# Kernel optimization log

Hardware: AMD Instinct MI355X
Metric: run time of the kernel (lower is better)

Reference implementation:

```python
import jax, jax.numpy as jnp
import numpy as np

DIM = 512
HEADS = 8
D_HEAD = 64
INNER_FF = 4 * DIM  # 2048
EPS = 1e-5
SCALE = D_HEAD ** -0.5


def _layernorm(x, w, b):
    x = x.astype(jnp.float32)
    mu = jnp.mean(x, axis=-1, keepdims=True)
    var = jnp.mean(jnp.square(x - mu), axis=-1, keepdims=True)
    return (x - mu) * jax.lax.rsqrt(var + EPS) * w + b


def _l2_attn(x, wq, bq, wv, bv, wo, bo):
    # x: [B, N, DIM]. k = q (context is ignored in the original module).
    b, n, _ = x.shape
    q = (x @ wq + bq).reshape(b, n, HEADS, D_HEAD).transpose(0, 2, 1, 3)  # b h n d
    v = (x @ wv + bv).reshape(b, n, HEADS, D_HEAD).transpose(0, 2, 1, 3)
    q = q.astype(jnp.float32)
    AB = jnp.einsum('bhid,bhjd->bhij', q, q)          # [b,h,n,n]
    AA = jnp.sum(jnp.square(q), axis=-1)               # [b,h,n]
    sim = -(AA[..., :, None] - 2.0 * AB + AA[..., None, :]) * SCALE
    attn = jax.nn.softmax(sim, axis=-1)
    out = jnp.einsum('bhij,bhjd->bhid', attn, v)       # [b,h,n,d]
    out = out.transpose(0, 2, 1, 3).reshape(b, n, HEADS * D_HEAD)
    return out @ wo + bo


def _geglu_ff(x, w1, b1, w2, b2):
    h = x @ w1 + b1                      # [B, N, 2*INNER_FF]
    a, gate = jnp.split(h, 2, axis=-1)
    return (a * jax.nn.gelu(gate, approximate=False)) @ w2 + b2


def setup_inputs() -> dict:
    key = jax.random.key(0)
    ks = jax.random.split(key, 24)
    s = 0.02
    d = {'x': jax.random.normal(ks[0], (4, 2048, DIM), jnp.float32)}
    # layernorms
    d['sa_norm_w'] = jnp.ones((DIM,), jnp.float32)
    d['sa_norm_b'] = jnp.zeros((DIM,), jnp.float32)
    d['ca_norm_w'] = jnp.ones((DIM,), jnp.float32)
    d['ca_norm_b'] = jnp.zeros((DIM,), jnp.float32)
    d['ff_norm_w'] = jnp.ones((DIM,), jnp.float32)
    d['ff_norm_b'] = jnp.zeros((DIM,), jnp.float32)
    # attn1 (self)
    d['a1_wq'] = jax.random.normal(ks[1], (DIM, DIM), jnp.float32) * s
    d['a1_bq'] = jnp.zeros((DIM,), jnp.float32)
    d['a1_wv'] = jax.random.normal(ks[2], (DIM, DIM), jnp.float32) * s
    d['a1_bv'] = jnp.zeros((DIM,), jnp.float32)
    d['a1_wo'] = jax.random.normal(ks[3], (DIM, DIM), jnp.float32) * s
    d['a1_bo'] = jnp.zeros((DIM,), jnp.float32)
    # attn2 (cross, but k=q and v from x in original code)
    d['a2_wq'] = jax.random.normal(ks[4], (DIM, DIM), jnp.float32) * s
    d['a2_bq'] = jnp.zeros((DIM,), jnp.float32)
    d['a2_wv'] = jax.random.normal(ks[5], (DIM, DIM), jnp.float32) * s
    d['a2_bv'] = jnp.zeros((DIM,), jnp.float32)
    d['a2_wo'] = jax.random.normal(ks[6], (DIM, DIM), jnp.float32) * s
    d['a2_bo'] = jnp.zeros((DIM,), jnp.float32)
    # GEGLU FFN
    d['ff_w1'] = jax.random.normal(ks[7], (DIM, 2 * INNER_FF), jnp.float32) * s
    d['ff_b1'] = jnp.zeros((2 * INNER_FF,), jnp.float32)
    d['ff_w2'] = jax.random.normal(ks[8], (INNER_FF, DIM), jnp.float32) * s
    d['ff_b2'] = jnp.zeros((DIM,), jnp.float32)
    return d


def reference(x, sa_norm_w, sa_norm_b, ca_norm_w, ca_norm_b, ff_norm_w, ff_norm_b,
              a1_wq, a1_bq, a1_wv, a1_bv, a1_wo, a1_bo,
              a2_wq, a2_bq, a2_wv, a2_bv, a2_wo, a2_bo,
              ff_w1, ff_b1, ff_w2, ff_b2):
    x = _l2_attn(_layernorm(x, sa_norm_w, sa_norm_b), a1_wq, a1_bq, a1_wv, a1_bv, a1_wo, a1_bo) + x
    x = _l2_attn(_layernorm(x, ca_norm_w, ca_norm_b), a2_wq, a2_bq, a2_wv, a2_bv, a2_wo, a2_bo) + x
    x = _geglu_ff(_layernorm(x, ff_norm_w, ff_norm_b), ff_w1, ff_b1, ff_w2, ff_b2) + x
    return x
```

## Files before the change

### kernel.cpp

```cpp
#include <hip/hip_runtime.h>
#include <hip/hip_bf16.h>


typedef short bf16x8 __attribute__((ext_vector_type(8)));
typedef float f32x4 __attribute__((ext_vector_type(4)));
typedef unsigned short u16;
typedef unsigned int u32;

__device__ __forceinline__ float bf2f(u16 u) {
    return __uint_as_float(((u32)u) << 16);
}
__device__ __forceinline__ u16 f2bf(float f) {
    u32 u = __float_as_uint(f);
    u32 rb = ((u >> 16) & 1u) + 0x7fffu;
    return (u16)((u + rb) >> 16);
}
__device__ __forceinline__ float gelu_fast(float x) {
    float y = 1.5957691216f * (x + 0.044715f * x * x * x);
    return x / (1.f + __expf(-y));
}
__device__ __forceinline__ void gl2lds16(const u16* g, u16* l) {
    __builtin_amdgcn_global_load_lds(
        (const __attribute__((address_space(1))) void*)(unsigned long long)(uintptr_t)g,
        (__attribute__((address_space(3))) void*)(unsigned long long)(uintptr_t)l,
        16, 0, 0);
}

struct TArgs {
    const float* src[8];
    u16* dst[8];
    int R[8], C[8];
    int start[9];
};
__global__ __launch_bounds__(256) void transpose_multi(TArgs a) {
    __shared__ float tile[32][33];
    int bid = blockIdx.x;
    int s = 0;
    while (bid >= a.start[s + 1]) s++;
    int local = bid - a.start[s];
    int R = a.R[s], C = a.C[s];
    int tx = C >> 5;
    int bx = local % tx, by = local / tx;
    const float* in = a.src[s];
    u16* out = a.dst[s];
    int t = threadIdx.x;
    int c = t & 31, r0 = (t >> 5) * 4;
#pragma unroll
    for (int i = 0; i < 4; i++)
        tile[r0 + i][c] = in[(size_t)(by * 32 + r0 + i) * C + bx * 32 + c];
    __syncthreads();
#pragma unroll
    for (int i = 0; i < 4; i++)
        out[(size_t)(bx * 32 + r0 + i) * R + by * 32 + c] = f2bf(tile[c][r0 + i]);
}

__global__ __launch_bounds__(256) void ln_kernel(const float* __restrict__ x,
                                                 const float* __restrict__ w,
                                                 const float* __restrict__ b,
                                                 u16* __restrict__ out) {
    int t = threadIdx.x;
    int wave = t >> 6, lane = t & 63;
    int row = blockIdx.x * 4 + wave;
    const float* xr = x + (size_t)row * 512 + lane * 8;
    float4 v0 = *(const float4*)xr;
    float4 v1 = *(const float4*)(xr + 4);
    float s1 = (v0.x + v0.y) + (v0.z + v0.w) + (v1.x + v1.y) + (v1.z + v1.w);
    float s2 = (v0.x * v0.x + v0.y * v0.y) + (v0.z * v0.z + v0.w * v0.w) +
               (v1.x * v1.x + v1.y * v1.y) + (v1.z * v1.z + v1.w * v1.w);
#pragma unroll
    for (int m = 1; m < 64; m <<= 1) {
        s1 += __shfl_xor(s1, m);
        s2 += __shfl_xor(s2, m);
    }
    float mu = s1 * (1.f / 512.f);
    float var = s2 * (1.f / 512.f) - mu * mu;
    float rs = rsqrtf(var + 1e-5f);
    const float* wp = w + lane * 8;
    const float* bp = b + lane * 8;
    float4 w0 = *(const float4*)wp;
    float4 w1 = *(const float4*)(wp + 4);
    float4 b0 = *(const float4*)bp;
    float4 b1 = *(const float4*)(bp + 4);
    u16 r[8];
    r[0] = f2bf((v0.x - mu) * rs * w0.x + b0.x);
    r[1] = f2bf((v0.y - mu) * rs * w0.y + b0.y);
    r[2] = f2bf((v0.z - mu) * rs * w0.z + b0.z);
    r[3] = f2bf((v0.w - mu) * rs * w0.w + b0.w);
    r[4] = f2bf((v1.x - mu) * rs * w1.x + b1.x);
    r[5] = f2bf((v1.y - mu) * rs * w1.y + b1.y);
    r[6] = f2bf((v1.z - mu) * rs * w1.z + b1.z);
    r[7] = f2bf((v1.w - mu) * rs * w1.w + b1.w);
    *(uint4*)(out + (size_t)row * 512 + lane * 8) = *(uint4*)r;
}

__global__ __launch_bounds__(256) void gemm_ff1(const u16* __restrict__ A,
                                                const u16* __restrict__ BT,
                                                const float* __restrict__ bias,
                                                u16* __restrict__ gout,
                                                int K) {
    __shared__ u16 As[2][128 * 32];
    __shared__ u16 Bs[2][128 * 32];
    int t = threadIdx.x;
    int wave = t >> 6, lane = t & 63, quad = lane >> 4, l16 = lane & 15;
    int m0 = blockIdx.x * 128, n0 = blockIdx.y * 64;
    f32x4 aacc[2][4], gacc[2][4];
#pragma unroll
    for (int i = 0; i < 2; i++)
#pragma unroll
        for (int j = 0; j < 4; j++) {
            aacc[i][j] = (f32x4){0.f, 0.f, 0.f, 0.f};
            gacc[i][j] = (f32x4){0.f, 0.f, 0.f, 0.f};
        }
    const u16* Ag = A + (size_t)(m0 + wave * 32 + (lane >> 2)) * K + (lane & 3) * 8;
    int brow = (wave < 2) ? (n0 + wave * 32) : (2048 + n0 + (wave - 2) * 32);
    const u16* Bg = BT + (size_t)(brow + (lane >> 2)) * K + (lane & 3) * 8;
    int lo = wave * 32 * 32;
    const size_t rstep = (size_t)16 * K;
    gl2lds16(Ag, &As[0][lo]);
    gl2lds16(Ag + rstep, &As[0][lo + 16 * 32]);
    gl2lds16(Bg, &Bs[0][lo]);
    gl2lds16(Bg + rstep, &Bs[0][lo + 16 * 32]);
    int buf = 0;
    for (int k0 = 0; k0 < K; k0 += 32, buf ^= 1) {
        int kn = (k0 + 32 < K) ? (k0 + 32) : k0;
        int nb = buf ^ 1;
        asm volatile("s_waitcnt lgkmcnt(0)\n\ts_barrier" ::: "memory");
        gl2lds16(Ag + kn, &As[nb][lo]);
        gl2lds16(Ag + kn + rstep, &As[nb][lo + 16 * 32]);
        gl2lds16(Bg + kn, &Bs[nb][lo]);
        gl2lds16(Bg + kn + rstep, &Bs[nb][lo + 16 * 32]);
        asm volatile("s_waitcnt vmcnt(4)\n\ts_barrier" ::: "memory");
        bf16x8 a[2];
#pragma unroll
        for (int i = 0; i < 2; i++)
            a[i] = *(const bf16x8*)&As[buf][(wave * 32 + i * 16 + l16) * 32 + quad * 8];
#pragma unroll
        for (int j = 0; j < 4; j++) {
            bf16x8 ba = *(const bf16x8*)&Bs[buf][(j * 16 + l16) * 32 + quad * 8];
            bf16x8 bg = *(const bf16x8*)&Bs[buf][(64 + j * 16 + l16) * 32 + quad * 8];
#pragma unroll
            for (int i = 0; i < 2; i++) {
                aacc[i][j] = __builtin_amdgcn_mfma_f32_16x16x32_bf16(a[i], ba, aacc[i][j], 0, 0, 0);
                gacc[i][j] = __builtin_amdgcn_mfma_f32_16x16x32_bf16(a[i], bg, gacc[i][j], 0, 0, 0);
            }
        }
    }
    asm volatile("s_waitcnt vmcnt(0)" ::: "memory");
    int row_base = m0 + wave * 32 + quad * 4;
#pragma unroll
    for (int j = 0; j < 4; j++) {
        int col = n0 + j * 16 + l16;
        float ba = bias[col];
        float bg = bias[2048 + col];
#pragma unroll
        for (int i = 0; i < 2; i++) {
#pragma unroll
            for (int r = 0; r < 4; r++) {
                int row = row_base + i * 16 + r;
                float av = aacc[i][j][r] + ba;
                float gv = gacc[i][j][r] + bg;
                gout[(size_t)row * 2048 + col] = f2bf(av * gelu_fast(gv));
            }
        }
    }
}

__global__ __launch_bounds__(256) void gemm_qv(const u16* __restrict__ A,
                                               const u16* __restrict__ BT,
                                               const float* __restrict__ bias,
                                               const float* __restrict__ bias2,
                                               u16* __restrict__ outb,
                                               u16* __restrict__ outb2,
                                               float* __restrict__ aa,
                                               int K) {
    __shared__ u16 As[2][128 * 32];
    __shared__ u16 Bs[2][128 * 32];
    int t = threadIdx.x;
    int wave = t >> 6, lane = t & 63, quad = lane >> 4, l16 = lane & 15;
    int m0 = blockIdx.x * 128, n0 = blockIdx.y * 128;
    f32x4 acc[2][8];
#pragma unroll
    for (int i = 0; i < 2; i++)
#pragma unroll
        for (int j = 0; j < 8; j++) acc[i][j] = (f32x4){0.f, 0.f, 0.f, 0.f};
    const u16* Ag = A + (size_t)(m0 + wave * 32 + (lane >> 2)) * K + (lane & 3) * 8;
    const u16* Bg = BT + (size_t)(n0 + wave * 32 + (lane >> 2)) * K + (lane & 3) * 8;
    int lo = wave * 32 * 32;
    const size_t rstep = (size_t)16 * K;
    gl2lds16(Ag, &As[0][lo]);
    gl2lds16(Ag + rstep, &As[0][lo + 16 * 32]);
    gl2lds16(Bg, &Bs[0][lo]);
    gl2lds16(Bg + rstep, &Bs[0][lo + 16 * 32]);
    int buf = 0;
    for (int k0 = 0; k0 < K; k0 += 32, buf ^= 1) {
        int kn = (k0 + 32 < K) ? (k0 + 32) : k0;
        int nb = buf ^ 1;
        asm volatile("s_waitcnt lgkmcnt(0)\n\ts_barrier" ::: "memory");
        gl2lds16(Ag + kn, &As[nb][lo]);
        gl2lds16(Ag + kn + rstep, &As[nb][lo + 16 * 32]);
        gl2lds16(Bg + kn, &Bs[nb][lo]);
        gl2lds16(Bg + kn + rstep, &Bs[nb][lo + 16 * 32]);
        asm volatile("s_waitcnt vmcnt(4)\n\ts_barrier" ::: "memory");
        bf16x8 a[2];
#pragma unroll
        for (int i = 0; i < 2; i++)
            a[i] = *(const bf16x8*)&As[buf][(wave * 32 + i * 16 + l16) * 32 + quad * 8];
#pragma unroll
        for (int j = 0; j < 8; j++) {
            bf16x8 b = *(const bf16x8*)&Bs[buf][(j * 16 + l16) * 32 + quad * 8];
#pragma unroll
            for (int i = 0; i < 2; i++)
                acc[i][j] = __builtin_amdgcn_mfma_f32_16x16x32_bf16(a[i], b, acc[i][j], 0, 0, 0);
        }
    }
    asm volatile("s_waitcnt vmcnt(0)" ::: "memory");
    int row_base = m0 + wave * 32 + quad * 4;
    bool isq = (n0 < 512);
    float ssq[2][2][4];
#pragma unroll
    for (int jh = 0; jh < 2; jh++)
#pragma unroll
        for (int i = 0; i < 2; i++)
#pragma unroll
            for (int r = 0; r < 4; r++) ssq[jh][i][r] = 0.f;
#pragma unroll
    for (int j = 0; j < 8; j++) {
        int col = n0 + j * 16 + l16;
        float bv = isq ? bias[col] : bias2[col - 512];
        int jh = j >> 2;
#pragma unroll
        for (int i = 0; i < 2; i++) {
            int rowA = row_base + i * 16;
            if (isq) {
                int hh = col >> 6, d = col & 63;
#pragma unroll
                for (int r = 0; r < 4; r++) {
                    int row = rowA + r;
                    float v = acc[i][j][r] + bv;
                    ssq[jh][i][r] += v * v;
                    outb[((size_t)((row >> 11) * 8 + hh) * 2048 + (row & 2047)) * 64 + d] = f2bf(v);
                }
            } else {
                int c2 = col - 512;
                int hh = c2 >> 6, d = c2 & 63;
                int n = rowA & 2047;
                int a4 = (n >> 2) & 7;
                int ncol = (n & ~31) + ((a4 & 3) << 3) + ((a4 >> 2) << 2);
                u32 plo = (u32)f2bf(acc[i][j][0] + bv) | ((u32)f2bf(acc[i][j][1] + bv) << 16);
                u32 phi = (u32)f2bf(acc[i][j][2] + bv) | ((u32)f2bf(acc[i][j][3] + bv) << 16);
                uint2 pk; pk.x = plo; pk.y = phi;
                *(uint2*)&outb2[((size_t)((rowA >> 11) * 8 + hh) * 64 + d) * 2048 + ncol] = pk;
            }
        }
    }
    if (isq) {
#pragma unroll
        for (int jh = 0; jh < 2; jh++) {
            int hh = (n0 >> 6) + jh;
#pragma unroll
            for (int i = 0; i < 2; i++) {
#pragma unroll
                for (int r = 0; r < 4; r++) {
                    float s = ssq[jh][i][r];
                    s += __shfl_xor(s, 1); s += __shfl_xor(s, 2);
                    s += __shfl_xor(s, 4); s += __shfl_xor(s, 8);
                    if (l16 == 0) {
                        int row = row_base + i * 16 + r;
                        aa[(size_t)((row >> 11) * 8 + hh) * 2048 + (row & 2047)] = s * 0.18033688f;
                    }
                }
            }
        }
    }
}

template <int MODE>
__global__ __launch_bounds__(256) void gemm_rect(const u16* __restrict__ A,
                                                 const u16* __restrict__ BT,
                                                 const float* __restrict__ bias,
                                                 const float* __restrict__ res,
                                                 float* __restrict__ outf,
                                                 int M, int N, int K) {
    __shared__ u16 As[2][128 * 32];
    __shared__ u16 Bs[2][64 * 32];
    int t = threadIdx.x;
    int wave = t >> 6, lane = t & 63, quad = lane >> 4, l16 = lane & 15;
    int m0 = blockIdx.x * 128, n0 = blockIdx.y * 64;
    f32x4 acc[2][4];
#pragma unroll
    for (int i = 0; i < 2; i++)
#pragma unroll
        for (int j = 0; j < 4; j++) acc[i][j] = (f32x4){0.f, 0.f, 0.f, 0.f};
    const u16* Ag = A + (size_t)(m0 + wave * 32 + (lane >> 2)) * K + (lane & 3) * 8;
    const u16* Bg = BT + (size_t)(n0 + wave * 16 + (lane >> 2)) * K + (lane & 3) * 8;
    int loA = wave * 32 * 32;
    int loB = wave * 16 * 32;
    const size_t rstep = (size_t)16 * K;
    gl2lds16(Ag, &As[0][loA]);
    gl2lds16(Ag + rstep, &As[0][loA + 16 * 32]);
    gl2lds16(Bg, &Bs[0][loB]);
    int buf = 0;
    for (int k0 = 0; k0 < K; k0 += 32, buf ^= 1) {
        int kn = (k0 + 32 < K) ? (k0 + 32) : k0;
        int nb = buf ^ 1;
        asm volatile("s_waitcnt lgkmcnt(0)\n\ts_barrier" ::: "memory");
        gl2lds16(Ag + kn, &As[nb][loA]);
        gl2lds16(Ag + kn + rstep, &As[nb][loA + 16 * 32]);
        gl2lds16(Bg + kn, &Bs[nb][loB]);
        asm volatile("s_waitcnt vmcnt(3)\n\ts_barrier" ::: "memory");
        bf16x8 a[2], b[4];
#pragma unroll
        for (int i = 0; i < 2; i++)
            a[i] = *(const bf16x8*)&As[buf][(wave * 32 + i * 16 + l16) * 32 + quad * 8];
#pragma unroll
        for (int j = 0; j < 4; j++)
            b[j] = *(const bf16x8*)&Bs[buf][(j * 16 + l16) * 32 + quad * 8];
#pragma unroll
        for (int i = 0; i < 2; i++)
#pragma unroll
            for (int j = 0; j < 4; j++)
                acc[i][j] = __builtin_amdgcn_mfma_f32_16x16x32_bf16(a[i], b[j], acc[i][j], 0, 0, 0);
    }
    asm volatile("s_waitcnt vmcnt(0)" ::: "memory");
    int row_base = m0 + wave * 32 + quad * 4;
#pragma unroll
    for (int j = 0; j < 4; j++) {
        int col = n0 + j * 16 + l16;
        float bv = bias[col];
#pragma unroll
        for (int i = 0; i < 2; i++) {
            int rowA = row_base + i * 16;
#pragma unroll
            for (int r = 0; r < 4; r++) {
                size_t idx = (size_t)(rowA + r) * N + col;
                outf[idx] = acc[i][j][r] + bv + res[idx];
            }
        }
    }
}

__global__ __launch_bounds__(256) void attn_mfma(const u16* __restrict__ qbuf,
                                                 const u16* __restrict__ vtp,
                                                 const float* __restrict__ aas,
                                                 u16* __restrict__ out) {
    __shared__ u16 L[2][16384];
    int bid = blockIdx.x;
    int bh = bid & 31;
    int itile = bid >> 5;
    const u16* qb = qbuf + (size_t)bh * 2048 * 64;
    const u16* vtb = vtp + (size_t)bh * 64 * 2048;
    const float* aab = aas + (size_t)bh * 2048;
    int t = threadIdx.x;
    int wave = t >> 6, lane = t & 63, quad = lane >> 4, l16 = lane & 15;
    int sw7 = l16 & 7;
    int ibase = itile * 128 + wave * 32;

    bf16x8 qf[2][2];
    f32x4 O[2][4];
    float lr[2] = {0.f, 0.f};
#pragma unroll
    for (int st = 0; st < 2; st++) {
        const u16* qr = qb + (size_t)(ibase + st * 16 + l16) * 64;
        qf[st][0] = *(const bf16x8*)(qr + quad * 8);
        qf[st][1] = *(const bf16x8*)(qr + 32 + quad * 8);
#pragma unroll
        for (int nt = 0; nt < 4; nt++) O[st][nt] = (f32x4){0.f, 0.f, 0.f, 0.f};
    }

    int qrow[4], qcs[4], qwof[4], vrow[4], vsl[4], vwof[4];
#pragma unroll
    for (int k = 0; k < 4; k++) {
        int s = t + k * 256;
        qrow[k] = s >> 3; qcs[k] = s & 7;
        qwof[k] = qrow[k] * 64 + 8 * (qcs[k] ^ (qrow[k] & 7));
        vrow[k] = s >> 4; vsl[k] = s & 15;
        vwof[k] = 8192 + vrow[k] * 128 + 8 * ((vsl[k] & 8) | ((vsl[k] & 7) ^ (vrow[k] & 7)));
    }
#pragma unroll
    for (int k = 0; k < 4; k++) {
        *(uint4*)&L[0][qwof[k]] = *(const uint4*)(qb + (size_t)qrow[k] * 64 + qcs[k] * 8);
        *(uint4*)&L[0][vwof[k]] = *(const uint4*)(vtb + (size_t)vrow[k] * 2048 + vsl[k] * 8);
    }
    __syncthreads();

    const float C0 = 0.36067376f;
    for (int it = 0; it < 16; ++it) {
        int cur = it & 1;
        int j0 = it << 7;
        uint4 pq[4], pv[4];
        bool more = (it + 1 < 16);
        if (more) {
            int j0n = j0 + 128;
#pragma unroll
            for (int k = 0; k < 4; k++) {
                pq[k] = *(const uint4*)(qb + (size_t)(j0n + qrow[k]) * 64 + qcs[k] * 8);
                pv[k] = *(const uint4*)(vtb + (size_t)vrow[k] * 2048 + j0n + vsl[k] * 8);
            }
        }
        const u16* Q = &L[cur][0];
        const u16* V = &L[cur][8192];
#pragma unroll
        for (int c = 0; c < 4; c++) {
            int r10 = c * 32 + l16, r20 = c * 32 + 16 + l16;
            bf16x8 a10 = *(const bf16x8*)&Q[r10 * 64 + 8 * (quad ^ sw7)];
            bf16x8 a11 = *(const bf16x8*)&Q[r10 * 64 + 8 * ((4 + quad) ^ sw7)];
            bf16x8 a20 = *(const bf16x8*)&Q[r20 * 64 + 8 * (quad ^ sw7)];
            bf16x8 a21 = *(const bf16x8*)&Q[r20 * 64 + 8 * ((4 + quad) ^ sw7)];
            f32x4 s0[2], s1[2];
            __builtin_amdgcn_s_setprio(1);
#pragma unroll
            for (int st = 0; st < 2; st++) {
                f32x4 z = {0.f, 0.f, 0.f, 0.f};
                s0[st] = __builtin_amdgcn_mfma_f32_16x16x32_bf16(a10, qf[st][0], z, 0, 0, 0);
                s0[st] = __builtin_amdgcn_mfma_f32_16x16x32_bf16(a11, qf[st][1], s0[st], 0, 0, 0);
                s1[st] = __builtin_amdgcn_mfma_f32_16x16x32_bf16(a20, qf[st][0], z, 0, 0, 0);
                s1[st] = __builtin_amdgcn_mfma_f32_16x16x32_bf16(a21, qf[st][1], s1[st], 0, 0, 0);
            }
            __builtin_amdgcn_s_setprio(0);
            float4 aav0 = *(const float4*)(aab + j0 + c * 32 + quad * 4);
            float4 aav1 = *(const float4*)(aab + j0 + c * 32 + 16 + quad * 4);
            bf16x8 pa[2];
#pragma unroll
            for (int st = 0; st < 2; st++) {
                float p0 = __builtin_amdgcn_exp2f(fmaf(s0[st][0], C0, -aav0.x));
                float p1 = __builtin_amdgcn_exp2f(fmaf(s0[st][1], C0, -aav0.y));
                float p2 = __builtin_amdgcn_exp2f(fmaf(s0[st][2], C0, -aav0.z));
                float p3 = __builtin_amdgcn_exp2f(fmaf(s0[st][3], C0, -aav0.w));
                float p4 = __builtin_amdgcn_exp2f(fmaf(s1[st][0], C0, -aav1.x));
                float p5 = __builtin_amdgcn_exp2f(fmaf(s1[st][1], C0, -aav1.y));
                float p6 = __builtin_amdgcn_exp2f(fmaf(s1[st][2], C0, -aav1.z));
                float p7 = __builtin_amdgcn_exp2f(fmaf(s1[st][3], C0, -aav1.w));
                lr[st] += (p0 + p1 + p2 + p3) + (p4 + p5 + p6 + p7);
                u32* pu = (u32*)&pa[st];
                pu[0] = __builtin_amdgcn_perm(__float_as_uint(p1), __float_as_uint(p0), 0x07060302u);
                pu[1] = __builtin_amdgcn_perm(__float_as_uint(p3), __float_as_uint(p2), 0x07060302u);
                pu[2] = __builtin_amdgcn_perm(__float_as_uint(p5), __float_as_uint(p4), 0x07060302u);
                pu[3] = __builtin_amdgcn_perm(__float_as_uint(p7), __float_as_uint(p6), 0x07060302u);
            }
            __builtin_amdgcn_s_setprio(1);
#pragma unroll
            for (int nt = 0; nt < 4; nt++) {
                int sl = c * 4 + quad;
                bf16x8 vf = *(const bf16x8*)&V[(nt * 16 + l16) * 128 + 8 * ((sl & 8) | ((sl & 7) ^ sw7))];
                O[0][nt] = __builtin_amdgcn_mfma_f32_16x16x32_bf16(pa[0], vf, O[0][nt], 0, 0, 0);
                O[1][nt] = __builtin_amdgcn_mfma_f32_16x16x32_bf16(pa[1], vf, O[1][nt], 0, 0, 0);
            }
            __builtin_amdgcn_s_setprio(0);
        }
        if (more) {
            u16* D = &L[cur ^ 1][0];
#pragma unroll
            for (int k = 0; k < 4; k++) {
                *(uint4*)&D[qwof[k]] = pq[k];
                *(uint4*)&D[vwof[k]] = pv[k];
            }
        }
        __syncthreads();
    }

    int b = bh >> 3, h = bh & 7;
#pragma unroll
    for (int st = 0; st < 2; st++) {
        float l = lr[st];
        l += __shfl_xor(l, 16);
        l += __shfl_xor(l, 32);
        float inv = 1.f / l;
#pragma unroll
        for (int r = 0; r < 4; r++) {
            float invr = __shfl(inv, quad * 4 + r);
            size_t row = (size_t)(b * 2048 + ibase + st * 16 + quad * 4 + r);
            u16* o = out + row * 512 + h * 64 + l16;
            o[0]  = f2bf(O[st][0][r] * invr);
            o[16] = f2bf(O[st][1][r] * invr);
            o[32] = f2bf(O[st][2][r] * invr);
            o[48] = f2bf(O[st][3][r] * invr);
        }
    }
}

extern "C" void kernel_launch(void* const* d_in, const int* in_sizes, int n_in,
                              void* d_out, int out_size, void* d_ws, size_t ws_size,
                              hipStream_t stream) {
    const float* x      = (const float*)d_in[0];
    const float* sa_w   = (const float*)d_in[1];
    const float* sa_b   = (const float*)d_in[2];
    const float* ca_w   = (const float*)d_in[3];
    const float* ca_b   = (const float*)d_in[4];
    const float* ffn_w  = (const float*)d_in[5];
    const float* ffn_b  = (const float*)d_in[6];
    const float* a1_wq  = (const float*)d_in[7];
    const float* a1_bq  = (const float*)d_in[8];
    const float* a1_wv  = (const float*)d_in[9];
    const float* a1_bv  = (const float*)d_in[10];
    const float* a1_wo  = (const float*)d_in[11];
    const float* a1_bo  = (const float*)d_in[12];
    const float* a2_wq  = (const float*)d_in[13];
    const float* a2_bq  = (const float*)d_in[14];
    const float* a2_wv  = (const float*)d_in[15];
    const float* a2_bv  = (const float*)d_in[16];
    const float* a2_wo  = (const float*)d_in[17];
    const float* a2_bo  = (const float*)d_in[18];
    const float* ff_w1  = (const float*)d_in[19];
    const float* ff_b1  = (const float*)d_in[20];
    const float* ff_w2  = (const float*)d_in[21];
    const float* ff_b2  = (const float*)d_in[22];

    char* ws = (char*)d_ws;
    const size_t MB = 1ull << 20;
    float* x_res   = (float*)(ws);
    u16* xn        = (u16*)(ws + 16 * MB);
    u16* wT_a1qv   = (u16*)(ws + 24 * MB);
    u16* wT_a2qv   = (u16*)(ws + 25 * MB);
    u16* wT_a1o    = (u16*)(ws + 26 * MB);
    u16* wT_a2o    = (u16*)(ws + 26 * MB + 512 * 1024);
    u16* wT_ff1    = (u16*)(ws + 27 * MB);
    u16* wT_ff2    = (u16*)(ws + 31 * MB);
    u16* qbuf      = (u16*)(ws + 34 * MB);
    u16* vtp       = (u16*)(ws + 42 * MB);
    float* aab     = (float*)(ws + 50 * MB);
    u16* attn_o    = (u16*)(ws + 51 * MB);
    u16* gbuf      = (u16*)(ws + 60 * MB);

    (void)in_sizes; (void)n_in; (void)out_size; (void)ws_size;

    TArgs ta;
    ta.src[0] = a1_wq; ta.dst[0] = wT_a1qv;               ta.R[0] = 512;  ta.C[0] = 512;
    ta.src[1] = a1_wv; ta.dst[1] = wT_a1qv + 512 * 512;   ta.R[1] = 512;  ta.C[1] = 512;
    ta.src[2] = a2_wq; ta.dst[2] = wT_a2qv;               ta.R[2] = 512;  ta.C[2] = 512;
    ta.src[3] = a2_wv; ta.dst[3] = wT_a2qv + 512 * 512;   ta.R[3] = 512;  ta.C[3] = 512;
    ta.src[4] = a1_wo; ta.dst[4] = wT_a1o;                ta.R[4] = 512;  ta.C[4] = 512;
    ta.src[5] = a2_wo; ta.dst[5] = wT_a2o;                ta.R[5] = 512;  ta.C[5] = 512;
    ta.src[6] = ff_w1; ta.dst[6] = wT_ff1;                ta.R[6] = 512;  ta.C[6] = 4096;
    ta.src[7] = ff_w2; ta.dst[7] = wT_ff2;                ta.R[7] = 2048; ta.C[7] = 512;
    ta.start[0] = 0;
    for (int s = 0; s < 8; s++)
        ta.start[s + 1] = ta.start[s] + (ta.C[s] >> 5) * (ta.R[s] >> 5);
    transpose_multi<<<ta.start[8], 256, 0, stream>>>(ta);

    ln_kernel<<<2048, 256, 0, stream>>>(x, sa_w, sa_b, xn);
    gemm_qv<<<dim3(64, 8), 256, 0, stream>>>(xn, wT_a1qv, a1_bq, a1_bv, qbuf, vtp, aab, 512);
    attn_mfma<<<512, 256, 0, stream>>>(qbuf, vtp, aab, attn_o);
    gemm_rect<2><<<dim3(64, 8), 256, 0, stream>>>(attn_o, wT_a1o, a1_bo, x, x_res, 8192, 512, 512);

    ln_kernel<<<2048, 256, 0, stream>>>(x_res, ca_w, ca_b, xn);
    gemm_qv<<<dim3(64, 8), 256, 0, stream>>>(xn, wT_a2qv, a2_bq, a2_bv, qbuf, vtp, aab, 512);
    attn_mfma<<<512, 256, 0, stream>>>(qbuf, vtp, aab, attn_o);
    gemm_rect<2><<<dim3(64, 8), 256, 0, stream>>>(attn_o, wT_a2o, a2_bo, x_res, x_res, 8192, 512, 512);

    ln_kernel<<<2048, 256, 0, stream>>>(x_res, ffn_w, ffn_b, xn);
    gemm_ff1<<<dim3(64, 32), 256, 0, stream>>>(xn, wT_ff1, ff_b1, gbuf, 512);
    gemm_rect<2><<<dim3(64, 8), 256, 0, stream>>>(gbuf, wT_ff2, ff_b2, x_res, (float*)d_out, 8192, 512, 2048);
}
```

Baseline: 381.6 us.

## Software-pipeline QK MFMAs across chunks and compute softmax row sums via MFMA

```diff
diff --git a/kernel.cpp b/kernel.cpp
--- a/kernel.cpp
+++ b/kernel.cpp
@@ -357,14 +357,20 @@
 
     bf16x8 qf[2][2];
     f32x4 O[2][4];
-    float lr[2] = {0.f, 0.f};
+    f32x4 sacc[2];
 #pragma unroll
     for (int st = 0; st < 2; st++) {
         const u16* qr = qb + (size_t)(ibase + st * 16 + l16) * 64;
         qf[st][0] = *(const bf16x8*)(qr + quad * 8);
         qf[st][1] = *(const bf16x8*)(qr + 32 + quad * 8);
+        sacc[st] = (f32x4){0.f, 0.f, 0.f, 0.f};
 #pragma unroll
         for (int nt = 0; nt < 4; nt++) O[st][nt] = (f32x4){0.f, 0.f, 0.f, 0.f};
+    }
+    bf16x8 vones;
+    {
+        u32* vo = (u32*)&vones;
+        vo[0] = vo[1] = vo[2] = vo[3] = 0x3F803F80u;
     }
 
     int qrow[4], qcs[4], qwof[4], vrow[4], vsl[4], vwof[4];
@@ -399,38 +405,43 @@
         }
         const u16* Q = &L[cur][0];
         const u16* V = &L[cur][8192];
-#pragma unroll
-        for (int c = 0; c < 4; c++) {
+
+        auto QK = [&](int c, f32x4 s0o[2], f32x4 s1o[2]) {
             int r10 = c * 32 + l16, r20 = c * 32 + 16 + l16;
             bf16x8 a10 = *(const bf16x8*)&Q[r10 * 64 + 8 * (quad ^ sw7)];
             bf16x8 a11 = *(const bf16x8*)&Q[r10 * 64 + 8 * ((4 + quad) ^ sw7)];
             bf16x8 a20 = *(const bf16x8*)&Q[r20 * 64 + 8 * (quad ^ sw7)];
             bf16x8 a21 = *(const bf16x8*)&Q[r20 * 64 + 8 * ((4 + quad) ^ sw7)];
-            f32x4 s0[2], s1[2];
             __builtin_amdgcn_s_setprio(1);
 #pragma unroll
             for (int st = 0; st < 2; st++) {
                 f32x4 z = {0.f, 0.f, 0.f, 0.f};
-                s0[st] = __builtin_amdgcn_mfma_f32_16x16x32_bf16(a10, qf[st][0], z, 0, 0, 0);
-                s0[st] = __builtin_amdgcn_mfma_f32_16x16x32_bf16(a11, qf[st][1], s0[st], 0, 0, 0);
-                s1[st] = __builtin_amdgcn_mfma_f32_16x16x32_bf16(a20, qf[st][0], z, 0, 0, 0);
-                s1[st] = __builtin_amdgcn_mfma_f32_16x16x32_bf16(a21, qf[st][1], s1[st], 0, 0, 0);
+                s0o[st] = __builtin_amdgcn_mfma_f32_16x16x32_bf16(a10, qf[st][0], z, 0, 0, 0);
+                s0o[st] = __builtin_amdgcn_mfma_f32_16x16x32_bf16(a11, qf[st][1], s0o[st], 0, 0, 0);
+                s1o[st] = __builtin_amdgcn_mfma_f32_16x16x32_bf16(a20, qf[st][0], z, 0, 0, 0);
+                s1o[st] = __builtin_amdgcn_mfma_f32_16x16x32_bf16(a21, qf[st][1], s1o[st], 0, 0, 0);
             }
             __builtin_amdgcn_s_setprio(0);
+        };
+
+        f32x4 sc0[2], sc1[2], sn0[2], sn1[2];
+        QK(0, sc0, sc1);
+#pragma unroll
+        for (int c = 0; c < 4; c++) {
+            if (c < 3) QK(c + 1, sn0, sn1);
             float4 aav0 = *(const float4*)(aab + j0 + c * 32 + quad * 4);
             float4 aav1 = *(const float4*)(aab + j0 + c * 32 + 16 + quad * 4);
             bf16x8 pa[2];
 #pragma unroll
             for (int st = 0; st < 2; st++) {
-                float p0 = __builtin_amdgcn_exp2f(fmaf(s0[st][0], C0, -aav0.x));
-                float p1 = __builtin_amdgcn_exp2f(fmaf(s0[st][1], C0, -aav0.y));
-                float p2 = __builtin_amdgcn_exp2f(fmaf(s0[st][2], C0, -aav0.z));
-                float p3 = __builtin_amdgcn_exp2f(fmaf(s0[st][3], C0, -aav0.w));
-                float p4 = __builtin_amdgcn_exp2f(fmaf(s1[st][0], C0, -aav1.x));
-                float p5 = __builtin_amdgcn_exp2f(fmaf(s1[st][1], C0, -aav1.y));
-                float p6 = __builtin_amdgcn_exp2f(fmaf(s1[st][2], C0, -aav1.z));
-                float p7 = __builtin_amdgcn_exp2f(fmaf(s1[st][3], C0, -aav1.w));
-                lr[st] += (p0 + p1 + p2 + p3) + (p4 + p5 + p6 + p7);
+                float p0 = __builtin_amdgcn_exp2f(fmaf(sc0[st][0], C0, -aav0.x));
+                float p1 = __builtin_amdgcn_exp2f(fmaf(sc0[st][1], C0, -aav0.y));
+                float p2 = __builtin_amdgcn_exp2f(fmaf(sc0[st][2], C0, -aav0.z));
+                float p3 = __builtin_amdgcn_exp2f(fmaf(sc0[st][3], C0, -aav0.w));
+                float p4 = __builtin_amdgcn_exp2f(fmaf(sc1[st][0], C0, -aav1.x));
+                float p5 = __builtin_amdgcn_exp2f(fmaf(sc1[st][1], C0, -aav1.y));
+                float p6 = __builtin_amdgcn_exp2f(fmaf(sc1[st][2], C0, -aav1.z));
+                float p7 = __builtin_amdgcn_exp2f(fmaf(sc1[st][3], C0, -aav1.w));
                 u32* pu = (u32*)&pa[st];
                 pu[0] = __builtin_amdgcn_perm(__float_as_uint(p1), __float_as_uint(p0), 0x07060302u);
                 pu[1] = __builtin_amdgcn_perm(__float_as_uint(p3), __float_as_uint(p2), 0x07060302u);
@@ -445,7 +456,11 @@
                 O[0][nt] = __builtin_amdgcn_mfma_f32_16x16x32_bf16(pa[0], vf, O[0][nt], 0, 0, 0);
                 O[1][nt] = __builtin_amdgcn_mfma_f32_16x16x32_bf16(pa[1], vf, O[1][nt], 0, 0, 0);
             }
+            sacc[0] = __builtin_amdgcn_mfma_f32_16x16x32_bf16(pa[0], vones, sacc[0], 0, 0, 0);
+            sacc[1] = __builtin_amdgcn_mfma_f32_16x16x32_bf16(pa[1], vones, sacc[1], 0, 0, 0);
             __builtin_amdgcn_s_setprio(0);
+#pragma unroll
+            for (int st = 0; st < 2; st++) { sc0[st] = sn0[st]; sc1[st] = sn1[st]; }
         }
         if (more) {
             u16* D = &L[cur ^ 1][0];
@@ -461,13 +476,9 @@
     int b = bh >> 3, h = bh & 7;
 #pragma unroll
     for (int st = 0; st < 2; st++) {
-        float l = lr[st];
-        l += __shfl_xor(l, 16);
-        l += __shfl_xor(l, 32);
-        float inv = 1.f / l;
 #pragma unroll
         for (int r = 0; r < 4; r++) {
-            float invr = __shfl(inv, quad * 4 + r);
+            float invr = 1.f / sacc[st][r];
             size_t row = (size_t)(b * 2048 + ibase + st * 16 + quad * 4 + r);
             u16* o = out + row * 512 + h * 64 + l16;
             o[0]  = f2bf(O[st][0][r] * invr);
```

Measured after the change: 387.8 us. No clear change (+1.6%).
